# Performance work log

Measured on AMD Instinct MI355X. Metric: run time of the kernel, lower is better.

Reference implementation:

```python
import jax, jax.numpy as jnp
import numpy as np

WINDOW = 20  # local attention window, per create_sparse_mask


def _make_mask(rng, n, sparsity_ratio=0.1):
    # local band: |i - j| <= window//2 (covers start/end clamping and the diagonal)
    idx = jnp.arange(n)
    mask = jnp.abs(idx[:, None] - idx[None, :]) <= (WINDOW // 2)
    # random edges: n_random (i, j) pairs set to 1 (duplicates harmless)
    n_random = int(sparsity_ratio * n * n)
    k1, k2 = jax.random.split(rng)
    ri = jax.random.randint(k1, (n_random,), 0, n)
    rj = jax.random.randint(k2, (n_random,), 0, n)
    mask = mask.at[ri, rj].set(True)
    return mask  # [n, n] bool


def setup_inputs() -> dict:
    rng = jax.random.key(0)
    kq, kk, kv, km = jax.random.split(rng, 4)
    B, H, S, D = 1, 8, 4096, 32
    return {
        "query": jax.random.normal(kq, (B, H, S, D), dtype=jnp.float32),
        "key": jax.random.normal(kk, (B, H, S, D), dtype=jnp.float32),
        "value": jax.random.normal(kv, (B, H, S, D), dtype=jnp.float32),
        "mask": _make_mask(km, S, sparsity_ratio=0.1),
    }


def reference(query, key, value, mask):
    # query/key/value: [B, H, S, D]; mask: [S, S] bool (True = attend)
    head_dim = query.shape[-1]
    scale = 1.0 / jnp.sqrt(jnp.float32(head_dim))
    scores = jnp.einsum("bhqd,bhkd->bhqk", query, key) * scale
    # torch: scores = scores * mask; masked_fill(mask == 0, -inf) -> equivalent to where
    scores = jnp.where(mask[None, None, :, :], scores, -jnp.inf)
    attn = jax.nn.softmax(scores, axis=-1)
    attn = jnp.nan_to_num(attn, nan=0.0)
    return jnp.einsum("bhqk,bhkd->bhqd", attn, value)
```

## Files before the change

kernel.cpp:

```cpp
#include <hip/hip_runtime.h>
#include <hip/hip_bf16.h>


#define S_  4096
#define D_  32
#define H_  8

typedef _Float16 half8 __attribute__((ext_vector_type(8)));
typedef __fp16 fp16x2 __attribute__((ext_vector_type(2)));
typedef short short8 __attribute__((ext_vector_type(8)));
typedef short short4v __attribute__((ext_vector_type(4)));
typedef float float4v __attribute__((ext_vector_type(4)));
typedef unsigned short ushort_t;
typedef unsigned int u32;

#if __has_builtin(__builtin_amdgcn_exp2f)
#define EXP2(x) __builtin_amdgcn_exp2f(x)
#else
#define EXP2(x) exp2f(x)
#endif

__device__ inline ushort_t f2h(float x) {
    union { _Float16 h; ushort_t u; } c; c.h = (_Float16)x; return c.u;
}

__global__ __launch_bounds__(256)
void prep_all(const float* __restrict__ Q, const float* __restrict__ K,
              const float* __restrict__ V, const int* __restrict__ mask,
              ushort_t* __restrict__ Qh, ushort_t* __restrict__ Kt,
              ushort_t* __restrict__ Vt, ushort_t* __restrict__ mlane)
{
    __shared__ u32 msh[16 * 257];
    const int bx = blockIdx.x;
    const int tid = threadIdx.x;
    union U8 { ushort_t u[8]; short8 v; };

    if (bx < 512) {
        const int e0 = (bx * 256 + tid) * 8;
        const float c = 0.17677669529663687f * 1.4426950408889634f;
        float4 a = *(const float4*)(Q + e0);
        float4 b = *(const float4*)(Q + e0 + 4);
        float f[8] = {a.x*c, a.y*c, a.z*c, a.w*c, b.x*c, b.y*c, b.z*c, b.w*c};
        U8 o;
#pragma unroll
        for (int i = 0; i < 8; ++i) o.u[i] = f2h(f[i]);
        *(short8*)(Qh + e0) = o.v;
    } else if (bx < 1024) {
        const int e0 = ((bx - 512) * 256 + tid) * 8;
        const int n = (e0 >> 3) & 15, quad = (e0 >> 7) & 3, t16 = (e0 >> 9) & 3;
        const int kt = (e0 >> 11) & 63, h = e0 >> 17;
        const int krow = kt * 64 + t16 * 16 + n;
        const float* src = K + ((size_t)h * S_ + krow) * D_ + quad * 8;
        float4 a = *(const float4*)src;
        float4 b = *(const float4*)(src + 4);
        float f[8] = {a.x, a.y, a.z, a.w, b.x, b.y, b.z, b.w};
        U8 o;
#pragma unroll
        for (int i = 0; i < 8; ++i) o.u[i] = f2h(f[i]);
        *(short8*)(Kt + e0) = o.v;
    } else if (bx < 1536) {
        const int e0 = ((bx - 1024) * 256 + tid) * 8;
        const int n = (e0 >> 3) & 15, quad = (e0 >> 7) & 3;
        const int dhalf = (e0 >> 9) & 1, khalf = (e0 >> 10) & 1;
        const int kt = (e0 >> 11) & 63, h = e0 >> 17;
        const int d = dhalf * 16 + n;
        U8 o;
#pragma unroll
        for (int j = 0; j < 8; ++j) {
            int krow = kt * 64 + khalf * 32 + (j >> 2) * 16 + quad * 4 + (j & 3);
            o.u[j] = f2h(V[((size_t)h * S_ + krow) * D_ + d]);
        }
        *(short8*)(Vt + e0) = o.v;
    } else {
        const int mb = bx - 1536;
        const int qt16 = mb >> 2, cc = mb & 3;
#pragma unroll
        for (int i = 0; i < 16; ++i) {
            int4 m4 = *(const int4*)(mask + (size_t)(qt16 * 16 + i) * S_ + cc * 1024 + tid * 4);
            u32 v = (m4.x != 0 ? 1u : 0u) | (m4.y != 0 ? 0x100u : 0u)
                  | (m4.z != 0 ? 0x10000u : 0u) | (m4.w != 0 ? 0x1000000u : 0u);
            msh[i * 257 + tid] = v;
        }
        __syncthreads();
        const int kt_local = tid >> 4, g = tid & 15;
        const int qd = g >> 2, n4 = g & 3;
        u32 o16[4] = {0, 0, 0, 0};
#pragma unroll
        for (int t16 = 0; t16 < 4; ++t16) {
            const int cbase = kt_local * 16 + t16 * 4 + qd;
#pragma unroll
            for (int b = 0; b < 4; ++b) {
                u32 v = msh[(n4 * 4 + b) * 257 + cbase];
                u32 nib = ((v * 0x01020408u) >> 24) & 0xFu;
                o16[b] |= nib << (t16 * 4);
            }
        }
        union { u32 w2[2]; short4v s; } pk;
        pk.w2[0] = o16[0] | (o16[1] << 16);
        pk.w2[1] = o16[2] | (o16[3] << 16);
        const int kt = cc * 16 + kt_local;
        *(short4v*)(mlane + ((size_t)(qt16 * 64 + kt) * 64 + g * 4)) = pk.s;
    }
}


__device__ inline void gl_lds16(const ushort_t* g, ushort_t* l) {
    __builtin_amdgcn_global_load_lds((const __attribute__((address_space(1))) void*)g,
                                     (__attribute__((address_space(3))) void*)l,
                                     16, 0, 0);
}

__global__ __launch_bounds__(512, 2)
void attn_mfma(const ushort_t* __restrict__ Qh, const ushort_t* __restrict__ Kt,
               const ushort_t* __restrict__ Vt, const ushort_t* __restrict__ mlane,
               float* __restrict__ out)
{
    __shared__ __align__(16) ushort_t sm[16384];
    ushort_t* K_s  = sm;
    ushort_t* Vt_s = sm + 8192;

    const int bid = blockIdx.x;
    const int swz = (bid & 7) * 64 + (bid >> 3);
    const int h  = swz >> 6;
    const int qb = swz & 63;
    const int q0 = qb * 64;

    const int tid = threadIdx.x;
    const int w = tid >> 6, l = tid & 63;
    const int half = w >> 2, wl = w & 3;
    const int n16 = l & 15, quad = l >> 4;

    const int qt16_u = __builtin_amdgcn_readfirstlane(qb * 4 + wl);
    const ushort_t* mlw = mlane + ((size_t)qt16_u << 12);

    const int qrow = q0 + wl * 16 + n16;
    const half8 qh = *(const half8*)(Qh + ((size_t)h * S_ + qrow) * D_ + quad * 8);

    half8 ones;
#pragma unroll
    for (int i = 0; i < 8; ++i) ones[i] = (_Float16)1.0f;

    float4v o0 = {0.f, 0.f, 0.f, 0.f};
    float4v o1 = {0.f, 0.f, 0.f, 0.f};
    float4v lacc = {0.f, 0.f, 0.f, 0.f};

    const int hb = half * 4096;
    const int kt_base = half * 32;

    {
        const size_t tb = ((size_t)(h * 64 + kt_base)) * 2048 + wl * 512 + l * 8;
        gl_lds16(Kt + tb, K_s  + hb + wl * 512);
        gl_lds16(Vt + tb, Vt_s + hb + wl * 512);
    }
    __syncthreads();

    for (int i = 0; i < 32; ++i) {
        const int kt = kt_base + i;
        const int cb = hb + (i & 1) * 2048;
        if (i < 31) {
            const int nb = hb + ((i + 1) & 1) * 2048;
            const size_t tb = ((size_t)(h * 64 + kt + 1)) * 2048 + wl * 512 + l * 8;
            gl_lds16(Kt + tb, K_s  + nb + wl * 512);
            gl_lds16(Vt + tb, Vt_s + nb + wl * 512);
        }

        const u32 ml = mlw[kt * 64 + l];

        float pv[4][4];
#pragma unroll
        for (int t16 = 0; t16 < 4; ++t16) {
            const half8 kb = *(const half8*)(K_s + cb + (t16 * 4 + quad) * 128 + n16 * 8);
            float4v c = {0.f, 0.f, 0.f, 0.f};
            c = __builtin_amdgcn_mfma_f32_16x16x32_f16(kb, qh, c, 0, 0, 0);
#pragma unroll
            for (int r = 0; r < 4; ++r) {
                float e = EXP2(c[r]);
                const int bp = t16 * 4 + r;
                u32 keep = (u32)((int)(ml << (31 - bp)) >> 31);
                pv[t16][r] = __uint_as_float(__float_as_uint(e) & keep);
            }
        }

#pragma unroll
        for (int kh = 0; kh < 2; ++kh) {
            union { fp16x2 hh[4]; half8 h8; } pk;
            pk.hh[0] = __builtin_amdgcn_cvt_pkrtz(pv[2*kh][0],   pv[2*kh][1]);
            pk.hh[1] = __builtin_amdgcn_cvt_pkrtz(pv[2*kh][2],   pv[2*kh][3]);
            pk.hh[2] = __builtin_amdgcn_cvt_pkrtz(pv[2*kh+1][0], pv[2*kh+1][1]);
            pk.hh[3] = __builtin_amdgcn_cvt_pkrtz(pv[2*kh+1][2], pv[2*kh+1][3]);
            const half8 pa = pk.h8;
            const half8 v0 = *(const half8*)(Vt_s + cb + ((kh * 2 + 0) * 4 + quad) * 128 + n16 * 8);
            const half8 v1 = *(const half8*)(Vt_s + cb + ((kh * 2 + 1) * 4 + quad) * 128 + n16 * 8);
            o0   = __builtin_amdgcn_mfma_f32_16x16x32_f16(pa, v0,   o0,   0, 0, 0);
            o1   = __builtin_amdgcn_mfma_f32_16x16x32_f16(pa, v1,   o1,   0, 0, 0);
            lacc = __builtin_amdgcn_mfma_f32_16x16x32_f16(pa, ones, lacc, 0, 0, 0);
        }

        __syncthreads();
    }

    float* red = (float*)sm;
    const int RSTR = 16 * 33 + 16;
    if (half == 1) {
        float* ro = red + wl * RSTR;
#pragma unroll
        for (int reg = 0; reg < 4; ++reg) {
            const int r = quad * 4 + reg;
            ro[r * 33 + n16]      = o0[reg];
            ro[r * 33 + 16 + n16] = o1[reg];
            if (n16 == 0) ro[16 * 33 + r] = lacc[reg];
        }
    }
    __syncthreads();
    if (half == 0) {
        const float* ro = red + wl * RSTR;
#pragma unroll
        for (int reg = 0; reg < 4; ++reg) {
            const int r = quad * 4 + reg;
            const float inv = 1.0f / (lacc[reg] + ro[16 * 33 + r]);
            const int row = q0 + wl * 16 + r;
            float* orow = out + ((size_t)h * S_ + row) * D_;
            orow[n16]      = (o0[reg] + ro[r * 33 + n16]) * inv;
            orow[16 + n16] = (o1[reg] + ro[r * 33 + 16 + n16]) * inv;
        }
    }
}


#define QT 64
#define KT 64
#define NSUB 4
#define KPT 16

__global__ __launch_bounds__(256, 2)
void sparse_attn_fp32(const float* __restrict__ Q, const float* __restrict__ K,
                      const float* __restrict__ V, const int* __restrict__ mask,
                      float* __restrict__ out)
{
    __shared__ float Ks[KT][D_];
    __shared__ float Vs[KT][D_];
    __shared__ float red_o[NSUB][QT][D_ + 1];
    __shared__ float red_l[NSUB][QT];

    const int h = blockIdx.y;
    const int q0 = blockIdx.x * QT;
    const int tid = threadIdx.x;
    const int ql = tid & 63;
    const int sub = tid >> 6;
    const int q = q0 + ql;
    const float scale = 0.17677669529663687f;

    float4 qreg[8];
    const float4* qrow = (const float4*)(Q + ((size_t)h * S_ + q) * D_);
#pragma unroll
    for (int i = 0; i < 8; ++i) qreg[i] = qrow[i];

    float o[D_];
#pragma unroll
    for (int d = 0; d < D_; ++d) o[d] = 0.f;
    float lsum0 = 0.f;

    const float* Kh = K + (size_t)h * S_ * D_;
    const float* Vh = V + (size_t)h * S_ * D_;

    for (int jt = 0; jt < S_; jt += KT) {
        __syncthreads();
        {
            const float4* gK = (const float4*)(Kh + (size_t)jt * D_);
            const float4* gV = (const float4*)(Vh + (size_t)jt * D_);
            float4* sK = (float4*)&Ks[0][0];
            float4* sV = (float4*)&Vs[0][0];
            sK[tid] = gK[tid]; sK[tid + 256] = gK[tid + 256];
            sV[tid] = gV[tid]; sV[tid + 256] = gV[tid + 256];
        }
        __syncthreads();

        int4 m4[4];
        {
            const int4* mr = (const int4*)(mask + (size_t)q * S_ + jt + sub * KPT);
#pragma unroll
            for (int i = 0; i < 4; ++i) m4[i] = mr[i];
        }
        const int* mb = (const int*)m4;

#pragma unroll
        for (int kk = 0; kk < KPT; ++kk) {
            const int jl = sub * KPT + kk;
            const float4* krow = (const float4*)&Ks[jl][0];
            float s = 0.f;
#pragma unroll
            for (int i = 0; i < 8; ++i) {
                float4 kv = krow[i];
                s += qreg[i].x * kv.x + qreg[i].y * kv.y + qreg[i].z * kv.z + qreg[i].w * kv.w;
            }
            const float p = mb[kk] ? __expf(s * scale) : 0.f;
            lsum0 += p;
            const float4* vrow = (const float4*)&Vs[jl][0];
#pragma unroll
            for (int i = 0; i < 8; ++i) {
                float4 vv = vrow[i];
                o[i * 4 + 0] += p * vv.x;
                o[i * 4 + 1] += p * vv.y;
                o[i * 4 + 2] += p * vv.z;
                o[i * 4 + 3] += p * vv.w;
            }
        }
    }

#pragma unroll
    for (int d = 0; d < D_; ++d) red_o[sub][ql][d] = o[d];
    red_l[sub][ql] = lsum0;
    __syncthreads();

    const int eq = tid & 63;
    const int dg = tid >> 6;
    float acc[8];
#pragma unroll
    for (int i = 0; i < 8; ++i) acc[i] = 0.f;
    float lsum = 0.f;
#pragma unroll
    for (int s2 = 0; s2 < NSUB; ++s2) {
        lsum += red_l[s2][eq];
#pragma unroll
        for (int i = 0; i < 8; ++i) acc[i] += red_o[s2][eq][dg * 8 + i];
    }
    const float inv = 1.0f / lsum;
    float* orow = out + ((size_t)h * S_ + q0 + eq) * D_ + dg * 8;
#pragma unroll
    for (int i = 0; i < 8; ++i) orow[i] = acc[i] * inv;
}


extern "C" void kernel_launch(void* const* d_in, const int* in_sizes, int n_in,
                              void* d_out, int out_size, void* d_ws, size_t ws_size,
                              hipStream_t stream) {
    const float* Q = (const float*)d_in[0];
    const float* K = (const float*)d_in[1];
    const float* V = (const float*)d_in[2];
    const int* mask = (const int*)d_in[3];
    float* out = (float*)d_out;

    const size_t MB = 1024 * 1024;
    if (ws_size < 8 * MB) {
        dim3 grid(S_ / QT, H_);
        sparse_attn_fp32<<<grid, 256, 0, stream>>>(Q, K, V, mask, out);
        return;
    }

    char* ws = (char*)d_ws;
    ushort_t* Qh = (ushort_t*)(ws + 0 * MB);
    ushort_t* Kt = (ushort_t*)(ws + 2 * MB);
    ushort_t* Vt = (ushort_t*)(ws + 4 * MB);
    ushort_t* mlane = (ushort_t*)(ws + 6 * MB);

    prep_all<<<2560, 256, 0, stream>>>(Q, K, V, mask, Qh, Kt, Vt, mlane);
    attn_mfma<<<512, 512, 0, stream>>>(Qh, Kt, Vt, mlane, out);
}
```

Baseline: 140.4 us.

## Split key range across four wave groups per block instead of two

The attention kernel now launches 1024-thread blocks in which four groups of four waves each process a quarter of the key tiles (16 iterations instead of 32). Shared memory doubles to hold double-buffered K/V for four groups, and the final reduction sums partial outputs and row sums from three groups into group zero. The mask bit extraction also switches to a signed bitfield-extract builtin when it is available. This adds in-block parallelism to shorten the serial key loop, in exchange for larger blocks, more shared memory per block and a heavier reduction.

Result: no change. 139.7 us (-0.5%).

```diff
diff --git a/kernel.cpp b/kernel.cpp
--- a/kernel.cpp
+++ b/kernel.cpp
@@ -18,6 +18,12 @@
 #define EXP2(x) __builtin_amdgcn_exp2f(x)
 #else
 #define EXP2(x) exp2f(x)
+#endif
+
+#if __has_builtin(__builtin_amdgcn_sbfe)
+#define SEXT_BIT(v, b) ((u32)__builtin_amdgcn_sbfe((int)(v), (b), 1))
+#else
+#define SEXT_BIT(v, b) ((u32)(((int)((v) << (31 - (b)))) >> 31))
 #endif
 
 __device__ inline ushort_t f2h(float x) {
@@ -110,14 +116,14 @@
                                      16, 0, 0);
 }
 
-__global__ __launch_bounds__(512, 2)
+__global__ __launch_bounds__(1024, 8)
 void attn_mfma(const ushort_t* __restrict__ Qh, const ushort_t* __restrict__ Kt,
                const ushort_t* __restrict__ Vt, const ushort_t* __restrict__ mlane,
                float* __restrict__ out)
 {
-    __shared__ __align__(16) ushort_t sm[16384];
+    __shared__ __align__(16) ushort_t sm[32768];
     ushort_t* K_s  = sm;
-    ushort_t* Vt_s = sm + 8192;
+    ushort_t* Vt_s = sm + 16384;
 
     const int bid = blockIdx.x;
     const int swz = (bid & 7) * 64 + (bid >> 3);
@@ -127,7 +133,7 @@
 
     const int tid = threadIdx.x;
     const int w = tid >> 6, l = tid & 63;
-    const int half = w >> 2, wl = w & 3;
+    const int kq = w >> 2, wl = w & 3;
     const int n16 = l & 15, quad = l >> 4;
 
     const int qt16_u = __builtin_amdgcn_readfirstlane(qb * 4 + wl);
@@ -144,21 +150,21 @@
     float4v o1 = {0.f, 0.f, 0.f, 0.f};
     float4v lacc = {0.f, 0.f, 0.f, 0.f};
 
-    const int hb = half * 4096;
-    const int kt_base = half * 32;
+    const int gb = kq * 4096;
+    const int kt_base = kq * 16;
 
     {
         const size_t tb = ((size_t)(h * 64 + kt_base)) * 2048 + wl * 512 + l * 8;
-        gl_lds16(Kt + tb, K_s  + hb + wl * 512);
-        gl_lds16(Vt + tb, Vt_s + hb + wl * 512);
+        gl_lds16(Kt + tb, K_s  + gb + wl * 512);
+        gl_lds16(Vt + tb, Vt_s + gb + wl * 512);
     }
     __syncthreads();
 
-    for (int i = 0; i < 32; ++i) {
+    for (int i = 0; i < 16; ++i) {
         const int kt = kt_base + i;
-        const int cb = hb + (i & 1) * 2048;
-        if (i < 31) {
-            const int nb = hb + ((i + 1) & 1) * 2048;
+        const int cb = gb + (i & 1) * 2048;
+        if (i < 15) {
+            const int nb = gb + ((i + 1) & 1) * 2048;
             const size_t tb = ((size_t)(h * 64 + kt + 1)) * 2048 + wl * 512 + l * 8;
             gl_lds16(Kt + tb, K_s  + nb + wl * 512);
             gl_lds16(Vt + tb, Vt_s + nb + wl * 512);
@@ -175,8 +181,7 @@
 #pragma unroll
             for (int r = 0; r < 4; ++r) {
                 float e = EXP2(c[r]);
-                const int bp = t16 * 4 + r;
-                u32 keep = (u32)((int)(ml << (31 - bp)) >> 31);
+                u32 keep = SEXT_BIT(ml, t16 * 4 + r);
                 pv[t16][r] = __uint_as_float(__float_as_uint(e) & keep);
             }
         }
@@ -201,8 +206,8 @@
 
     float* red = (float*)sm;
     const int RSTR = 16 * 33 + 16;
-    if (half == 1) {
-        float* ro = red + wl * RSTR;
+    if (kq != 0) {
+        float* ro = red + ((kq - 1) * 4 + wl) * RSTR;
 #pragma unroll
         for (int reg = 0; reg < 4; ++reg) {
             const int r = quad * 4 + reg;
@@ -212,16 +217,23 @@
         }
     }
     __syncthreads();
-    if (half == 0) {
-        const float* ro = red + wl * RSTR;
+    if (kq == 0) {
 #pragma unroll
         for (int reg = 0; reg < 4; ++reg) {
             const int r = quad * 4 + reg;
-            const float inv = 1.0f / (lacc[reg] + ro[16 * 33 + r]);
+            float s0 = o0[reg], s1 = o1[reg], sl = lacc[reg];
+#pragma unroll
+            for (int p = 0; p < 3; ++p) {
+                const float* ro = red + (p * 4 + wl) * RSTR;
+                s0 += ro[r * 33 + n16];
+                s1 += ro[r * 33 + 16 + n16];
+                sl += ro[16 * 33 + r];
+            }
+            const float inv = 1.0f / sl;
             const int row = q0 + wl * 16 + r;
             float* orow = out + ((size_t)h * S_ + row) * D_;
-            orow[n16]      = (o0[reg] + ro[r * 33 + n16]) * inv;
-            orow[16 + n16] = (o1[reg] + ro[r * 33 + 16 + n16]) * inv;
+            orow[n16]      = s0 * inv;
+            orow[16 + n16] = s1 * inv;
         }
     }
 }
@@ -354,5 +366,5 @@
     ushort_t* mlane = (ushort_t*)(ws + 6 * MB);
 
     prep_all<<<2560, 256, 0, stream>>>(Q, K, V, mask, Qh, Kt, Vt, mlane);
-    attn_mfma<<<512, 512, 0, stream>>>(Qh, Kt, Vt, mlane, out);
-}
+    attn_mfma<<<512, 1024, 0, stream>>>(Qh, Kt, Vt, mlane, out);
+}
```
